# Kernel tuning notes

Measured on AMD Instinct MI355X. Metric: run time of the kernel, lower is better.

The kernel has to match this reference:

```python
import jax, jax.numpy as jnp
import numpy as np

B, N, H, E = 32, 8192, 128, 10

def setup_inputs() -> dict:
    key = jax.random.key(0)
    ks = jax.random.split(key, 16)
    nrm = lambda k, s: jax.random.normal(k, s, dtype=jnp.float32) * 0.05
    z = lambda s: jnp.zeros(s, dtype=jnp.float32)
    o = lambda s: jnp.ones(s, dtype=jnp.float32)
    return {
        'points': jax.random.normal(ks[0], (B, N, 3), dtype=jnp.float32),
        'category_ids': jax.random.randint(ks[1], (B,), 0, E, dtype=jnp.int32),
        'pr_w1': nrm(ks[2], (3, H)), 'pr_b1': z((H,)), 'pr_g1': o((H,)), 'pr_be1': z((H,)),
        'pr_w2': nrm(ks[3], (H, H)), 'pr_b2': z((H,)), 'pr_g2': o((H,)), 'pr_be2': z((H,)),
        'cat_emb': nrm(ks[4], (E, H)),
        'cr_w1': nrm(ks[5], (2 * H, H)), 'cr_b1': z((H,)), 'cr_g1': o((H,)), 'cr_be1': z((H,)),
        'cr_w2': nrm(ks[6], (H, H // 2)), 'cr_b2': z((H // 2,)), 'cr_g2': o((H // 2,)), 'cr_be2': z((H // 2,)),
        'cr_w3': nrm(ks[7], (H // 2, 3)), 'cr_b3': z((3,)),
        'sy_w1': nrm(ks[8], (3, H // 2)), 'sy_b1': z((H // 2,)), 'sy_g1': o((H // 2,)), 'sy_be1': z((H // 2,)),
        'sy_w2': nrm(ks[9], (H // 2, 3)), 'sy_b2': z((3,)),
        'sp_w1': nrm(ks[10], (E, 3, H)), 'sp_b1': z((E, H)), 'sp_g1': o((E, H)), 'sp_be1': z((E, H)),
        'sp_w2': nrm(ks[11], (E, H, H // 2)), 'sp_b2': z((E, H // 2)), 'sp_g2': o((E, H // 2)), 'sp_be2': z((E, H // 2)),
        'sp_w3': nrm(ks[12], (E, H // 2, 3)), 'sp_b3': z((E, 3)),
    }

def _ln(x, g, b):
    mu = jnp.mean(x, -1, keepdims=True)
    var = jnp.mean((x - mu) ** 2, -1, keepdims=True)
    return (x - mu) * jax.lax.rsqrt(var + 1e-5) * g + b

def _lrelu(x):
    return jnp.where(x >= 0, x, 0.2 * x)

def reference(points, category_ids,
              pr_w1, pr_b1, pr_g1, pr_be1, pr_w2, pr_b2, pr_g2, pr_be2,
              cat_emb,
              cr_w1, cr_b1, cr_g1, cr_be1, cr_w2, cr_b2, cr_g2, cr_be2, cr_w3, cr_b3,
              sy_w1, sy_b1, sy_g1, sy_be1, sy_w2, sy_b2,
              sp_w1, sp_b1, sp_g1, sp_be1, sp_w2, sp_b2, sp_g2, sp_be2, sp_w3, sp_b3):
    xyz = points[..., :3]
    # shared point refinement MLP
    pf = _lrelu(_ln(points @ pr_w1 + pr_b1, pr_g1, pr_be1))
    pf = _lrelu(_ln(pf @ pr_w2 + pr_b2, pr_g2, pr_be2))  # [B,N,H]
    ce = cat_emb[category_ids][:, None, :]  # [B,1,H]
    comb = jnp.concatenate([pf, jnp.broadcast_to(ce, pf.shape)], axis=-1)  # [B,N,2H]
    h = _lrelu(_ln(comb @ cr_w1 + cr_b1, cr_g1, cr_be1))
    h = _lrelu(_ln(h @ cr_w2 + cr_b2, cr_g2, cr_be2))
    offsets = h @ cr_w3 + cr_b3  # [B,N,3]
    # category-conditioned expert MLPs (MoE dispatch via per-sample gather)
    g = lambda p: p[category_ids]
    ph = jnp.einsum('bni,bio->bno', xyz, g(sp_w1)) + g(sp_b1)[:, None, :]
    ph = _lrelu(_ln(ph, g(sp_g1)[:, None, :], g(sp_be1)[:, None, :]))
    ph = jnp.einsum('bni,bio->bno', ph, g(sp_w2)) + g(sp_b2)[:, None, :]
    ph = _lrelu(_ln(ph, g(sp_g2)[:, None, :], g(sp_be2)[:, None, :]))
    prior = jnp.einsum('bni,bio->bno', ph, g(sp_w3)) + g(sp_b3)[:, None, :]
    offsets = offsets + 0.5 * prior
    # symmetry refinement for categories 2 and 8 (mirror x)
    flip = jnp.array([-1.0, 1.0, 1.0], dtype=points.dtype)
    mx = xyz * flip
    s = _lrelu(_ln(mx @ sy_w1 + sy_b1, sy_g1, sy_be1))
    s = (s @ sy_w2 + sy_b2) * flip
    mask = ((category_ids == 2) | (category_ids == 8))[:, None, None]
    offsets = jnp.where(mask, (offsets + s) * 0.5, offsets)
    return offsets
```

## Files before the change

### kernel.cpp

```cpp
#include <hip/hip_runtime.h>
#include <hip/hip_bf16.h>
#include <stdint.h>

typedef __attribute__((ext_vector_type(8))) short bf16x8;
typedef __attribute__((ext_vector_type(4))) float f32x4;

#define NT 256

#define WS_CE    0
#define WS_PR1   16384
#define WS_PR2   24576
#define WS_CR1   57344
#define WS_CR2   90112
#define WS_CR3   106496
#define WS_SY1   108544
#define WS_SY2   112640
#define WS_SP1   114688
#define WS_SP2   196608
#define WS_SP3   360448


__device__ __forceinline__ short bf1(float x) {
    unsigned u = __float_as_uint(x);
    return (short)((u + 0x7fffu + ((u >> 16) & 1u)) >> 16);
}
__device__ __forceinline__ float bfval(short h) {
    return __uint_as_float(((unsigned)(unsigned short)h) << 16);
}
__device__ __forceinline__ unsigned cvtpk(float lo, float hi) {
    unsigned r;
    asm("v_cvt_pk_bf16_f32 %0, %1, %2" : "=v"(r) : "v"(lo), "v"(hi));
    return r;
}

template<int CTRL>
__device__ __forceinline__ float dpp_add(float v) {
    int o = __builtin_amdgcn_mov_dpp(__float_as_int(v), CTRL, 0xf, 0xf, true);
    return v + __int_as_float(o);
}
__device__ __forceinline__ float row16_sum(float v) {
    v = dpp_add<0x128>(v);
    v = dpp_add<0x124>(v);
    v = dpp_add<0x122>(v);
    v = dpp_add<0x121>(v);
    return v;
}

template<int NF>
__device__ __forceinline__ void init_acc(f32x4* acc, const float* __restrict__ bias, int c) {
#pragma unroll
    for (int f = 0; f < NF; ++f) {
        const float bv = bias[f * 16 + c];
        acc[f]     = (f32x4){bv, bv, bv, bv};
        acc[8 + f] = (f32x4){bv, bv, bv, bv};
    }
}
__device__ __forceinline__ void init_b3(f32x4& a0, f32x4& a1, const float* __restrict__ b3, int c) {
    const float bv = (c < 3) ? b3[c] : 0.f;
    a0 = (f32x4){bv, bv, bv, bv};
    a1 = (f32x4){bv, bv, bv, bv};
}

__device__ __forceinline__ bf16x8 mkA6(float a0, float a1, float a2, bool active) {
    bf16x8 A = (bf16x8){0, 0, 0, 0, 0, 0, 0, 0};
    if (active) {
        const short h0 = bf1(a0), h1 = bf1(a1), h2 = bf1(a2);
        A[0] = h0; A[1] = h1; A[2] = h2;
        A[3] = bf1(a0 - bfval(h0));
        A[4] = bf1(a1 - bfval(h1));
        A[5] = bf1(a2 - bfval(h2));
    }
    return A;
}

template<int NF>
__device__ __forceinline__ void mfma_reg(bf16x8 A0, bf16x8 A1, const char* __restrict__ Bg,
                                         int lane, f32x4* acc) {
#pragma unroll
    for (int f = 0; f < NF; ++f) {
        bf16x8 B = *(const bf16x8*)(Bg + f * 1024 + lane * 16);
        acc[f]     = __builtin_amdgcn_mfma_f32_16x16x32_bf16(A0, B, acc[f], 0, 0, 0);
        acc[8 + f] = __builtin_amdgcn_mfma_f32_16x16x32_bf16(A1, B, acc[8 + f], 0, 0, 0);
    }
}

template<int NF, int KS>
__device__ __forceinline__ void mfma_lds(const char* actb, const char* __restrict__ Bg,
                                         int R0c, int g, int lane, f32x4* acc) {
    const int swz = (R0c & 7) << 4;
#pragma unroll
    for (int ks = 0; ks < KS; ++ks) {
        const int kb = ks * 64 + g * 16;
        bf16x8 A0 = *(const bf16x8*)(actb + ((R0c * 256 + kb) ^ swz));
        bf16x8 A1 = *(const bf16x8*)(actb + (((R0c + 16) * 256 + kb) ^ swz));
#pragma unroll
        for (int f = 0; f < NF; ++f) {
            bf16x8 B = *(const bf16x8*)(Bg + (f * KS + ks) * 1024 + lane * 16);
            acc[f]     = __builtin_amdgcn_mfma_f32_16x16x32_bf16(A0, B, acc[f], 0, 0, 0);
            acc[8 + f] = __builtin_amdgcn_mfma_f32_16x16x32_bf16(A1, B, acc[8 + f], 0, 0, 0);
        }
    }
}

__device__ __forceinline__ void mfma3(const char* actb, const char* __restrict__ Bg,
                                      int R0c, int g, int lane, f32x4& a0, f32x4& a1) {
    const int swz = (R0c & 7) << 4;
#pragma unroll
    for (int ks = 0; ks < 2; ++ks) {
        const int kb = ks * 64 + g * 16;
        bf16x8 A0 = *(const bf16x8*)(actb + ((R0c * 256 + kb) ^ swz));
        bf16x8 A1 = *(const bf16x8*)(actb + (((R0c + 16) * 256 + kb) ^ swz));
        bf16x8 B = *(const bf16x8*)(Bg + ks * 1024 + lane * 16);
        a0 = __builtin_amdgcn_mfma_f32_16x16x32_bf16(A0, B, a0, 0, 0, 0);
        a1 = __builtin_amdgcn_mfma_f32_16x16x32_bf16(A1, B, a1, 0, 0, 0);
    }
}

template<int NF>
__device__ __forceinline__ void ln_lrelu_frag(f32x4* acc, int c,
                                              const float* __restrict__ g,
                                              const float* __restrict__ be, float invN) {
    float gv[NF], bev[NF];
#pragma unroll
    for (int f = 0; f < NF; ++f) { gv[f] = g[f * 16 + c]; bev[f] = be[f * 16 + c]; }
#pragma unroll
    for (int rf = 0; rf < 2; ++rf) {
        f32x4 s1 = acc[rf * 8];
        f32x4 s2 = acc[rf * 8] * acc[rf * 8];
#pragma unroll
        for (int f = 1; f < NF; ++f) {
            s1 += acc[rf * 8 + f];
            s2 += acc[rf * 8 + f] * acc[rf * 8 + f];
        }
#pragma unroll
        for (int q = 0; q < 4; ++q) { s1[q] = row16_sum(s1[q]); s2[q] = row16_sum(s2[q]); }
        const f32x4 mu = s1 * invN;
        f32x4 ri;
#pragma unroll
        for (int q = 0; q < 4; ++q)
            ri[q] = rsqrtf(fmaf(s2[q], invN, -mu[q] * mu[q]) + 1e-5f);
#pragma unroll
        for (int f = 0; f < NF; ++f) {
            f32x4 x = (acc[rf * 8 + f] - mu) * ri;
            x = x * gv[f] + bev[f];
            acc[rf * 8 + f] = __builtin_elementwise_max(x, 0.2f * x);
        }
    }
}

template<int NF>
__device__ __forceinline__ void pack_store(char* dst, f32x4* acc, int R0, int c, int g) {
#pragma unroll
    for (int rf = 0; rf < 2; ++rf)
#pragma unroll
        for (int q = 0; q < 4; ++q) {
            const int row = R0 + rf * 16 + g * 4 + q;
            const int rbase = row * 256;
            const int swz = (row & 7) << 4;
#pragma unroll
            for (int m = 0; m < NF / 2; ++m) {
                const unsigned val = cvtpk(acc[rf * 8 + m][q], acc[rf * 8 + m + NF / 2][q]);
                *(unsigned*)(dst + ((rbase + (m * 16 + c) * 4) ^ swz)) = val;
            }
        }
}


__global__ void ce_precompute_kernel(const int* __restrict__ cats,
                                     const float* __restrict__ cat_emb,
                                     const float* __restrict__ cr_w1,
                                     const float* __restrict__ cr_b1,
                                     float* __restrict__ ce_out) {
    const int bb = blockIdx.x;
    const int j = threadIdx.x;
    const int c = cats[bb];
    float acc = cr_b1[j];
#pragma unroll 4
    for (int k = 0; k < 128; ++k)
        acc = fmaf(cat_emb[c * 128 + k], cr_w1[(128 + k) * 128 + j], acc);
    ce_out[bb * 128 + j] = acc;
}

__global__ void wfrag_kernel(
    const float* __restrict__ pr_w1, const float* __restrict__ pr_w2,
    const float* __restrict__ cr_w1, const float* __restrict__ cr_w2,
    const float* __restrict__ cr_w3, const float* __restrict__ sy_w1,
    const float* __restrict__ sy_w2, const float* __restrict__ sp_w1,
    const float* __restrict__ sp_w2, const float* __restrict__ sp_w3,
    char* __restrict__ ws)
{
    const int id = blockIdx.x * 256 + threadIdx.x;
    int local, KS, base, cat = 0;
    const float* W = nullptr;
    int mode;
    int Nstride = 0;

    if (id < 512)        { local = id;          KS = 1; base = WS_PR1; W = pr_w1; mode = 0; Nstride = 128; }
    else if (id < 2560)  { local = id - 512;    KS = 4; base = WS_PR2; W = pr_w2; mode = 1; Nstride = 128; }
    else if (id < 4608)  { local = id - 2560;   KS = 4; base = WS_CR1; W = cr_w1; mode = 1; Nstride = 128; }
    else if (id < 5632)  { local = id - 4608;   KS = 4; base = WS_CR2; W = cr_w2; mode = 1; Nstride = 64; }
    else if (id < 5760)  { local = id - 5632;   KS = 2; base = WS_CR3; W = cr_w3; mode = 2; }
    else if (id < 6016)  { local = id - 5760;   KS = 1; base = WS_SY1; W = sy_w1; mode = 0; Nstride = 64; }
    else if (id < 6144)  { local = id - 6016;   KS = 2; base = WS_SY2; W = sy_w2; mode = 2; }
    else if (id < 11264) { int r = id - 6144;  cat = r / 512;  local = r % 512;
                           KS = 1; base = WS_SP1 + cat * 8192;  W = sp_w1 + cat * 384;  mode = 0; Nstride = 128; }
    else if (id < 21504) { int r = id - 11264; cat = r / 1024; local = r % 1024;
                           KS = 4; base = WS_SP2 + cat * 16384; W = sp_w2 + cat * 8192; mode = 1; Nstride = 64; }
    else                 { int r = id - 21504; cat = r / 128;  local = r % 128;
                           KS = 2; base = WS_SP3 + cat * 2048;  W = sp_w3 + cat * 192;  mode = 2; }

    const int lane = local & 63;
    const int fk = local >> 6;
    const int ks = fk % KS;
    const int f = fk / KS;
    const int c = lane & 15;
    const int g = lane >> 4;
    const int n = f * 16 + c;
    const int p0 = ks * 32 + g * 8;

    bf16x8 H;
#pragma unroll
    for (int e = 0; e < 8; ++e) {
        const int p = p0 + e;
        float v = 0.f;
        if (mode == 0)      { if (p < 6) v = W[(p < 3 ? p : p - 3) * Nstride + n]; }
        else if (mode == 1) { const int k = (p >> 1) + (p & 1) * 64; v = W[k * Nstride + n]; }
        else                { const int k = (p >> 1) + (p & 1) * 32; if (n < 3) v = W[k * 3 + n]; }
        H[e] = bf1(v);
    }
    *(bf16x8*)(ws + base + local * 16) = H;
}


__global__ __launch_bounds__(NT, 3)
void shape_refine_mfma6(
    const float* __restrict__ points, const int* __restrict__ cats,
    const float* __restrict__ pr_b1, const float* __restrict__ pr_g1, const float* __restrict__ pr_be1,
    const float* __restrict__ pr_b2, const float* __restrict__ pr_g2, const float* __restrict__ pr_be2,
    const float* __restrict__ cr_g1, const float* __restrict__ cr_be1,
    const float* __restrict__ cr_b2, const float* __restrict__ cr_g2, const float* __restrict__ cr_be2,
    const float* __restrict__ cr_b3,
    const float* __restrict__ sy_b1, const float* __restrict__ sy_g1, const float* __restrict__ sy_be1,
    const float* __restrict__ sy_b2,
    const float* __restrict__ sp_b1, const float* __restrict__ sp_g1, const float* __restrict__ sp_be1,
    const float* __restrict__ sp_b2, const float* __restrict__ sp_g2, const float* __restrict__ sp_be2,
    const float* __restrict__ sp_b3,
    const char* __restrict__ ws,
    float* __restrict__ out)
{
    __shared__ char act[32768];

    const int t = threadIdx.x;
    const int lane = t & 63;
    const int wid = t >> 6;
    const int c = lane & 15;
    const int g = lane >> 4;
    const int R0 = wid * 32;
    const int R0c = R0 + c;

    const int bid = blockIdx.x;
    const int batch = bid >> 6;
    const int pbase = batch * 8192 + (bid & 63) * 128;

    const int cat = __builtin_amdgcn_readfirstlane(cats[batch]);
    const bool sym = (cat == 2) || (cat == 8);

    const float* p0 = points + 3 * (pbase + R0c);
    const float x0 = p0[0], x1 = p0[1], x2 = p0[2];
    const float y0 = p0[48], y1 = p0[49], y2 = p0[50];

    const bf16x8 A0 = mkA6(x0, x1, x2, g == 0);
    const bf16x8 A1 = mkA6(y0, y1, y2, g == 0);

    f32x4 acc[16];
    f32x4 ocr0, ocr1, oo0, oo1;

    init_acc<8>(acc, pr_b1, c);
    mfma_reg<8>(A0, A1, ws + WS_PR1, lane, acc);
    ln_lrelu_frag<8>(acc, c, pr_g1, pr_be1, 1.f / 128.f);
    pack_store<8>(act, acc, R0, c, g);

    init_acc<8>(acc, pr_b2, c);
    mfma_lds<8, 4>(act, ws + WS_PR2, R0c, g, lane, acc);
    ln_lrelu_frag<8>(acc, c, pr_g2, pr_be2, 1.f / 128.f);
    pack_store<8>(act, acc, R0, c, g);

    init_acc<8>(acc, (const float*)(ws + WS_CE) + batch * 128, c);
    mfma_lds<8, 4>(act, ws + WS_CR1, R0c, g, lane, acc);
    ln_lrelu_frag<8>(acc, c, cr_g1, cr_be1, 1.f / 128.f);
    pack_store<8>(act, acc, R0, c, g);

    init_acc<4>(acc, cr_b2, c);
    mfma_lds<4, 4>(act, ws + WS_CR2, R0c, g, lane, acc);
    ln_lrelu_frag<4>(acc, c, cr_g2, cr_be2, 1.f / 64.f);
    pack_store<4>(act, acc, R0, c, g);

    init_b3(ocr0, ocr1, cr_b3, c);
    mfma3(act, ws + WS_CR3, R0c, g, lane, ocr0, ocr1);

    init_acc<8>(acc, sp_b1 + cat * 128, c);
    mfma_reg<8>(A0, A1, ws + WS_SP1 + cat * 8192, lane, acc);
    ln_lrelu_frag<8>(acc, c, sp_g1 + cat * 128, sp_be1 + cat * 128, 1.f / 128.f);
    pack_store<8>(act, acc, R0, c, g);

    init_acc<4>(acc, sp_b2 + cat * 64, c);
    mfma_lds<4, 4>(act, ws + WS_SP2 + cat * 16384, R0c, g, lane, acc);
    ln_lrelu_frag<4>(acc, c, sp_g2 + cat * 64, sp_be2 + cat * 64, 1.f / 64.f);
    pack_store<4>(act, acc, R0, c, g);

    init_b3(oo0, oo1, sp_b3 + cat * 3, c);
    mfma3(act, ws + WS_SP3 + cat * 2048, R0c, g, lane, oo0, oo1);
    oo0 = ocr0 + 0.5f * oo0;
    oo1 = ocr1 + 0.5f * oo1;

    if (sym) {
        init_acc<4>(acc, sy_b1, c);
        const bf16x8 S0 = mkA6(-x0, x1, x2, g == 0);
        const bf16x8 S1 = mkA6(-y0, y1, y2, g == 0);
        mfma_reg<4>(S0, S1, ws + WS_SY1, lane, acc);
        ln_lrelu_frag<4>(acc, c, sy_g1, sy_be1, 1.f / 64.f);
        pack_store<4>(act, acc, R0, c, g);
        f32x4 s0, s1;
        init_b3(s0, s1, sy_b2, c);
        mfma3(act, ws + WS_SY2, R0c, g, lane, s0, s1);
        const float flip = (c == 0) ? -1.f : 1.f;
#pragma unroll
        for (int q = 0; q < 4; ++q) {
            oo0[q] = (oo0[q] + flip * s0[q]) * 0.5f;
            oo1[q] = (oo1[q] + flip * s1[q]) * 0.5f;
        }
    }

    if (c < 3) {
#pragma unroll
        for (int q = 0; q < 4; ++q) {
            const int row0 = R0 + g * 4 + q;
            out[3 * (pbase + row0) + c] = oo0[q];
            out[3 * (pbase + row0 + 16) + c] = oo1[q];
        }
    }
}


extern "C" void kernel_launch(void* const* d_in, const int* in_sizes, int n_in,
                              void* d_out, int out_size, void* d_ws, size_t ws_size,
                              hipStream_t stream) {
    const float* points  = (const float*)d_in[0];
    const int*   cats    = (const int*)  d_in[1];
    const float* pr_w1   = (const float*)d_in[2];
    const float* pr_b1   = (const float*)d_in[3];
    const float* pr_g1   = (const float*)d_in[4];
    const float* pr_be1  = (const float*)d_in[5];
    const float* pr_w2   = (const float*)d_in[6];
    const float* pr_b2   = (const float*)d_in[7];
    const float* pr_g2   = (const float*)d_in[8];
    const float* pr_be2  = (const float*)d_in[9];
    const float* cat_emb = (const float*)d_in[10];
    const float* cr_w1   = (const float*)d_in[11];
    const float* cr_b1   = (const float*)d_in[12];
    const float* cr_g1   = (const float*)d_in[13];
    const float* cr_be1  = (const float*)d_in[14];
    const float* cr_w2   = (const float*)d_in[15];
    const float* cr_b2   = (const float*)d_in[16];
    const float* cr_g2   = (const float*)d_in[17];
    const float* cr_be2  = (const float*)d_in[18];
    const float* cr_w3   = (const float*)d_in[19];
    const float* cr_b3   = (const float*)d_in[20];
    const float* sy_w1   = (const float*)d_in[21];
    const float* sy_b1   = (const float*)d_in[22];
    const float* sy_g1   = (const float*)d_in[23];
    const float* sy_be1  = (const float*)d_in[24];
    const float* sy_w2   = (const float*)d_in[25];
    const float* sy_b2   = (const float*)d_in[26];
    const float* sp_w1   = (const float*)d_in[27];
    const float* sp_b1   = (const float*)d_in[28];
    const float* sp_g1   = (const float*)d_in[29];
    const float* sp_be1  = (const float*)d_in[30];
    const float* sp_w2   = (const float*)d_in[31];
    const float* sp_b2   = (const float*)d_in[32];
    const float* sp_g2   = (const float*)d_in[33];
    const float* sp_be2  = (const float*)d_in[34];
    const float* sp_w3   = (const float*)d_in[35];
    const float* sp_b3   = (const float*)d_in[36];

    char* ws = (char*)d_ws;
    float* out = (float*)d_out;

    ce_precompute_kernel<<<dim3(32), dim3(128), 0, stream>>>(cats, cat_emb, cr_w1, cr_b1, (float*)ws);
    wfrag_kernel<<<dim3(89), dim3(256), 0, stream>>>(pr_w1, pr_w2, cr_w1, cr_w2, cr_w3,
                                                     sy_w1, sy_w2, sp_w1, sp_w2, sp_w3, ws);

    shape_refine_mfma6<<<dim3(2048), dim3(NT), 0, stream>>>(
        points, cats,
        pr_b1, pr_g1, pr_be1,
        pr_b2, pr_g2, pr_be2,
        cr_g1, cr_be1,
        cr_b2, cr_g2, cr_be2,
        cr_b3,
        sy_b1, sy_g1, sy_be1, sy_b2,
        sp_b1, sp_g1, sp_be1,
        sp_b2, sp_g2, sp_be2,
        sp_b3,
        ws, out);
}
```

Measured before the change: 96.28 us.

## Raise occupancy bound, prefetch A fragments, add setprio around MFMA loops

Raises the launch-bounds minimum from 3 to 4 blocks per CU, which pushes the compiler to cap registers so more waves can be resident. All A fragments are now loaded from LDS before the MFMA loops instead of being interleaved with them. s_setprio is raised around the MFMA sequences so matrix work gets scheduling priority. The LayerNorm normalize step is rewritten as a single fused multiply-add per element. The tighter register budget and the extra live fragments together risk register spills.

```diff
diff --git a/kernel.cpp b/kernel.cpp
--- a/kernel.cpp
+++ b/kernel.cpp
@@ -76,43 +76,55 @@
 template<int NF>
 __device__ __forceinline__ void mfma_reg(bf16x8 A0, bf16x8 A1, const char* __restrict__ Bg,
                                          int lane, f32x4* acc) {
+    __builtin_amdgcn_s_setprio(1);
 #pragma unroll
     for (int f = 0; f < NF; ++f) {
         bf16x8 B = *(const bf16x8*)(Bg + f * 1024 + lane * 16);
         acc[f]     = __builtin_amdgcn_mfma_f32_16x16x32_bf16(A0, B, acc[f], 0, 0, 0);
         acc[8 + f] = __builtin_amdgcn_mfma_f32_16x16x32_bf16(A1, B, acc[8 + f], 0, 0, 0);
     }
+    __builtin_amdgcn_s_setprio(0);
 }
 
 template<int NF, int KS>
 __device__ __forceinline__ void mfma_lds(const char* actb, const char* __restrict__ Bg,
                                          int R0c, int g, int lane, f32x4* acc) {
     const int swz = (R0c & 7) << 4;
+    bf16x8 Afr[2 * KS];
 #pragma unroll
     for (int ks = 0; ks < KS; ++ks) {
         const int kb = ks * 64 + g * 16;
-        bf16x8 A0 = *(const bf16x8*)(actb + ((R0c * 256 + kb) ^ swz));
-        bf16x8 A1 = *(const bf16x8*)(actb + (((R0c + 16) * 256 + kb) ^ swz));
+        Afr[2 * ks]     = *(const bf16x8*)(actb + ((R0c * 256 + kb) ^ swz));
+        Afr[2 * ks + 1] = *(const bf16x8*)(actb + (((R0c + 16) * 256 + kb) ^ swz));
+    }
+    __builtin_amdgcn_s_setprio(1);
+#pragma unroll
+    for (int ks = 0; ks < KS; ++ks) {
 #pragma unroll
         for (int f = 0; f < NF; ++f) {
             bf16x8 B = *(const bf16x8*)(Bg + (f * KS + ks) * 1024 + lane * 16);
-            acc[f]     = __builtin_amdgcn_mfma_f32_16x16x32_bf16(A0, B, acc[f], 0, 0, 0);
-            acc[8 + f] = __builtin_amdgcn_mfma_f32_16x16x32_bf16(A1, B, acc[8 + f], 0, 0, 0);
-        }
-    }
+            acc[f]     = __builtin_amdgcn_mfma_f32_16x16x32_bf16(Afr[2 * ks], B, acc[f], 0, 0, 0);
+            acc[8 + f] = __builtin_amdgcn_mfma_f32_16x16x32_bf16(Afr[2 * ks + 1], B, acc[8 + f], 0, 0, 0);
+        }
+    }
+    __builtin_amdgcn_s_setprio(0);
 }
 
 __device__ __forceinline__ void mfma3(const char* actb, const char* __restrict__ Bg,
                                       int R0c, int g, int lane, f32x4& a0, f32x4& a1) {
     const int swz = (R0c & 7) << 4;
+    bf16x8 Afr[4];
 #pragma unroll
     for (int ks = 0; ks < 2; ++ks) {
         const int kb = ks * 64 + g * 16;
-        bf16x8 A0 = *(const bf16x8*)(actb + ((R0c * 256 + kb) ^ swz));
-        bf16x8 A1 = *(const bf16x8*)(actb + (((R0c + 16) * 256 + kb) ^ swz));
+        Afr[2 * ks]     = *(const bf16x8*)(actb + ((R0c * 256 + kb) ^ swz));
+        Afr[2 * ks + 1] = *(const bf16x8*)(actb + (((R0c + 16) * 256 + kb) ^ swz));
+    }
+#pragma unroll
+    for (int ks = 0; ks < 2; ++ks) {
         bf16x8 B = *(const bf16x8*)(Bg + ks * 1024 + lane * 16);
-        a0 = __builtin_amdgcn_mfma_f32_16x16x32_bf16(A0, B, a0, 0, 0, 0);
-        a1 = __builtin_amdgcn_mfma_f32_16x16x32_bf16(A1, B, a1, 0, 0, 0);
+        a0 = __builtin_amdgcn_mfma_f32_16x16x32_bf16(Afr[2 * ks], B, a0, 0, 0, 0);
+        a1 = __builtin_amdgcn_mfma_f32_16x16x32_bf16(Afr[2 * ks + 1], B, a1, 0, 0, 0);
     }
 }
 
@@ -139,10 +151,11 @@
 #pragma unroll
         for (int q = 0; q < 4; ++q)
             ri[q] = rsqrtf(fmaf(s2[q], invN, -mu[q] * mu[q]) + 1e-5f);
+        const f32x4 nmuri = -mu * ri;
 #pragma unroll
         for (int f = 0; f < NF; ++f) {
-            f32x4 x = (acc[rf * 8 + f] - mu) * ri;
-            x = x * gv[f] + bev[f];
+            f32x4 xh = acc[rf * 8 + f] * ri + nmuri;
+            f32x4 x = xh * gv[f] + bev[f];
             acc[rf * 8 + f] = __builtin_elementwise_max(x, 0.2f * x);
         }
     }
@@ -232,8 +245,8 @@
 }
 
 
-__global__ __launch_bounds__(NT, 3)
-void shape_refine_mfma6(
+__global__ __launch_bounds__(NT, 4)
+void shape_refine_mfma8(
     const float* __restrict__ points, const int* __restrict__ cats,
     const float* __restrict__ pr_b1, const float* __restrict__ pr_g1, const float* __restrict__ pr_be1,
     const float* __restrict__ pr_b2, const float* __restrict__ pr_g2, const float* __restrict__ pr_be2,
@@ -390,7 +403,7 @@
     wfrag_kernel<<<dim3(89), dim3(256), 0, stream>>>(pr_w1, pr_w2, cr_w1, cr_w2, cr_w3,
                                                      sy_w1, sy_w2, sp_w1, sp_w2, sp_w3, ws);
 
-    shape_refine_mfma6<<<dim3(2048), dim3(NT), 0, stream>>>(
+    shape_refine_mfma8<<<dim3(2048), dim3(NT), 0, stream>>>(
         points, cats,
         pr_b1, pr_g1, pr_be1,
         pr_b2, pr_g2, pr_be2,
```

After: 147.2 us. +52.9%, slower.
